# Optimization experiments

Hardware: AMD Instinct MI355X
Metric: run time of the kernel (lower is better)

The kernel has to match this reference:

```python
import jax, jax.numpy as jnp
import numpy as np

N_NODES = 100_000
N_EDGES = 3_200_000
IN_DIM, HID_DIM, EMB_DIM = 128, 64, 32


def setup_inputs() -> dict:
    key = jax.random.key(0)
    k0, k1, k2, k3, k4, k5 = jax.random.split(key, 6)
    x = jax.random.normal(k0, (N_NODES, IN_DIM), dtype=jnp.float32)
    edge_index = jax.random.randint(k1, (2, N_EDGES), 0, N_NODES, dtype=jnp.int32)
    # GCNConv parameters (glorot-ish scale)
    W1 = jax.random.normal(k2, (IN_DIM, HID_DIM), dtype=jnp.float32) / np.sqrt(IN_DIM)
    b1 = jnp.zeros((HID_DIM,), dtype=jnp.float32)
    W2 = jax.random.normal(k3, (HID_DIM, EMB_DIM), dtype=jnp.float32) / np.sqrt(HID_DIM)
    b2 = jnp.zeros((EMB_DIM,), dtype=jnp.float32)
    return {"x": x, "W1": W1, "b1": b1, "W2": W2, "b2": b2, "edge_index": edge_index}


def reference(x, W1, b1, W2, b2, edge_index):
    """Two-layer GCN encoder (PyG GCNConv semantics, eval mode so dropout is a no-op).

    Each GCNConv: add self-loops, symmetric deg^-1/2 normalization,
    out = scatter_add(norm_e * (x @ W)[src], dst) + b.
    """
    N = x.shape[0]
    loops = jnp.arange(N, dtype=edge_index.dtype)
    src = jnp.concatenate([edge_index[0], loops])  # [E+N]
    dst = jnp.concatenate([edge_index[1], loops])  # [E+N]

    # degree of destination nodes (self-loops guarantee deg >= 1)
    deg = jax.ops.segment_sum(jnp.ones_like(dst, dtype=jnp.float32), dst,
                              num_segments=N)
    dinv = jax.lax.rsqrt(deg)                      # deg^-1/2, finite since deg>=1
    norm = dinv[src] * dinv[dst]                   # [E+N]

    def gcn_conv(h, W, b):
        h = h @ W                                  # dense transform [N, D_out]
        msg = h[src] * norm[:, None]               # gather + scale [E+N, D_out]
        return jax.ops.segment_sum(msg, dst, num_segments=N) + b

    h = jax.nn.relu(gcn_conv(x, W1, b1))
    # F.dropout with training=False is identity -> omitted
    return gcn_conv(h, W2, b2)
```

## Files before the change

kernel.cpp:

```cpp
#include <hip/hip_runtime.h>

static constexpr int NN = 100000;
static constexpr int NE = 3200000;
static constexpr int DI = 128;
static constexpr int DH = 64;
static constexpr int DO = 32;

static constexpr int NBK  = 391;
static constexpr int BCAP = 9216;
static constexpr int TILE = 4096;
static constexpr int NEB  = (NE + TILE - 1) / TILE;
static constexpr int XW1_BASE = NEB + 1;
static constexpr int XW1_BLOCKS = (NN + 63) / 64;

typedef short short8 __attribute__((ext_vector_type(8)));
typedef float f32x4  __attribute__((ext_vector_type(4)));

__device__ __forceinline__ unsigned short f2bf(float f) {
    union { float f; unsigned u; } v; v.f = f;
    unsigned r = v.u + 0x7FFFu + ((v.u >> 16) & 1u);
    return (unsigned short)(r >> 16);
}
__device__ __forceinline__ float bflo(unsigned u) {
    union { unsigned u; float f; } v; v.u = u << 16; return v.f;
}
__device__ __forceinline__ float bfhi(unsigned u) {
    union { unsigned u; float f; } v; v.u = u & 0xFFFF0000u; return v.f;
}

__global__ void k_zero(int* __restrict__ p, int n) {
    int i = blockIdx.x * blockDim.x + threadIdx.x;
    if (i < n) p[i] = 0;
}

__global__ __launch_bounds__(256) void k_mega(
        const int* __restrict__ src, const int* __restrict__ dst,
        int* __restrict__ bcur, int* __restrict__ bstore,
        const float* __restrict__ x, const float* __restrict__ W1,
        const float* __restrict__ W2,
        unsigned short* __restrict__ w2bf, unsigned short* __restrict__ h1b) {
    __shared__ int hist[NBK];
    __shared__ int lcur[NBK];
    __shared__ int gpos[NBK];
    __shared__ int stage[TILE];
    __shared__ unsigned short bid[TILE];

    int tid = threadIdx.x;

    if (blockIdx.x < NEB) {
        for (int i = tid; i < NBK; i += 256) hist[i] = 0;
        __syncthreads();

        int base = blockIdx.x * TILE;
        int rem = NE - base;
        int p[16]; unsigned short bb[16];
#pragma unroll
        for (int k4 = 0; k4 < 4; ++k4) {
            int off = tid * 16 + k4 * 4;
            if (off < rem) {
                int4 s4 = *(const int4*)(src + base + off);
                int4 d4 = *(const int4*)(dst + base + off);
                int k = 4 * k4;
                bb[k + 0] = (unsigned short)((unsigned)d4.x >> 8);
                p [k + 0] = ((d4.x & 255) << 24) | s4.x;
                atomicAdd(&hist[bb[k + 0]], 1);
                bb[k + 1] = (unsigned short)((unsigned)d4.y >> 8);
                p [k + 1] = ((d4.y & 255) << 24) | s4.y;
                atomicAdd(&hist[bb[k + 1]], 1);
                bb[k + 2] = (unsigned short)((unsigned)d4.z >> 8);
                p [k + 2] = ((d4.z & 255) << 24) | s4.z;
                atomicAdd(&hist[bb[k + 2]], 1);
                bb[k + 3] = (unsigned short)((unsigned)d4.w >> 8);
                p [k + 3] = ((d4.w & 255) << 24) | s4.w;
                atomicAdd(&hist[bb[k + 3]], 1);
            } else {
                int k = 4 * k4;
                bb[k + 0] = 0xFFFF; bb[k + 1] = 0xFFFF;
                bb[k + 2] = 0xFFFF; bb[k + 3] = 0xFFFF;
            }
        }
        __syncthreads();

        for (int i = tid; i < NBK; i += 256)
            gpos[i] = atomicAdd(&bcur[i], hist[i]);
        __syncthreads();

        if (tid < 64) {
            int carry = 0;
            for (int c = 0; c < (NBK + 63) / 64; ++c) {
                int idx = c * 64 + tid;
                int v = (idx < NBK) ? hist[idx] : 0;
                int inc = v;
#pragma unroll
                for (int o = 1; o < 64; o <<= 1) {
                    int u = __shfl_up(inc, o, 64);
                    if (tid >= o) inc += u;
                }
                int tot = __shfl(inc, 63, 64);
                if (idx < NBK) { int ex = carry + inc - v; hist[idx] = ex; lcur[idx] = ex; }
                carry += tot;
            }
        }
        __syncthreads();

#pragma unroll
        for (int k = 0; k < 16; ++k) {
            if (bb[k] != 0xFFFF) {
                int lp = atomicAdd(&lcur[bb[k]], 1);
                stage[lp] = p[k];
                bid[lp] = bb[k];
            }
        }
        __syncthreads();

        int tcnt = min(TILE, rem);
        for (int i = tid; i < tcnt; i += 256) {
            int b = bid[i];
            int off = gpos[b] + (i - hist[b]);
            if (off < BCAP) bstore[b * BCAP + off] = stage[i];
        }
    } else if (blockIdx.x == NEB) {
        for (int i = tid; i < DH * DO; i += 256) w2bf[i] = f2bf(W2[i]);
    } else {
        int wave = tid >> 6, lane = tid & 63;
        int q = lane >> 4, m = lane & 15, o0 = wave * 16;
        int nb = (blockIdx.x - XW1_BASE) * 64;

        short8 bfr[4];
#pragma unroll
        for (int kb = 0; kb < 4; ++kb)
#pragma unroll
            for (int j = 0; j < 8; ++j)
                bfr[kb][j] = (short)f2bf(W1[(kb * 32 + q * 8 + j) * DH + o0 + m]);

#pragma unroll
        for (int mt = 0; mt < 4; ++mt) {
            int row = min(nb + mt * 16 + m, NN - 1);
            const float* xr = x + (size_t)row * DI;
            f32x4 acc = {0.f, 0.f, 0.f, 0.f};
#pragma unroll
            for (int kb = 0; kb < 4; ++kb) {
                f32x4 u0 = *(const f32x4*)(xr + kb * 32 + q * 8);
                f32x4 u1 = *(const f32x4*)(xr + kb * 32 + q * 8 + 4);
                short8 a;
                a[0] = (short)f2bf(u0.x); a[1] = (short)f2bf(u0.y);
                a[2] = (short)f2bf(u0.z); a[3] = (short)f2bf(u0.w);
                a[4] = (short)f2bf(u1.x); a[5] = (short)f2bf(u1.y);
                a[6] = (short)f2bf(u1.z); a[7] = (short)f2bf(u1.w);
                acc = __builtin_amdgcn_mfma_f32_16x16x32_bf16(a, bfr[kb], acc, 0, 0, 0);
            }
#pragma unroll
            for (int r = 0; r < 4; ++r) {
                int n = nb + mt * 16 + q * 4 + r;
                if (n < NN) h1b[(size_t)n * DH + o0 + m] = f2bf(acc[r]);
            }
        }
    }
}

__global__ __launch_bounds__(512) void k_bsort(
        const int* __restrict__ bcur, int* __restrict__ bstore,
        int* __restrict__ rpb, int* __restrict__ rpe, float* __restrict__ dinv,
        unsigned* __restrict__ h1) {
    __shared__ int buf[BCAP];
    __shared__ int sorted[BCAP];
    __shared__ int hist[256], scan[256], cur[256];
    __shared__ float sdinv[256];

    int b = blockIdx.x, tid = threadIdx.x;
    int cnt = min(bcur[b], BCAP);
    int base = b * BCAP;
    for (int i = tid; i < cnt; i += 512) buf[i] = bstore[base + i];
    if (tid < 256) hist[tid] = 0;
    __syncthreads();
    for (int i = tid; i < cnt; i += 512)
        atomicAdd(&hist[((unsigned)buf[i]) >> 24], 1);
    __syncthreads();

    if (tid < 64) {
        int carry = 0;
        for (int c = 0; c < 4; ++c) {
            int idx = c * 64 + tid;
            int v = hist[idx];
            int inc = v;
#pragma unroll
            for (int o = 1; o < 64; o <<= 1) {
                int u = __shfl_up(inc, o, 64);
                if (tid >= o) inc += u;
            }
            int tot = __shfl(inc, 63, 64);
            scan[idx] = carry + inc - v;
            cur[idx]  = carry + inc - v;
            carry += tot;
        }
    }
    __syncthreads();

    if (tid < 256) {
        int n = b * 256 + tid;
        if (n < NN) {
            int beg = base + scan[tid];
            rpb[n] = beg;
            rpe[n] = beg + hist[tid];
            float dv = rsqrtf(1.0f + (float)hist[tid]);
            dinv[n] = dv;
            sdinv[tid] = dv;
        }
    }

    for (int i = tid; i < cnt; i += 512) {
        unsigned pv = (unsigned)buf[i];
        int pos = atomicAdd(&cur[pv >> 24], 1);
        sorted[pos] = (int)(pv & 0xFFFFFF);
    }
    __syncthreads();
    for (int i = tid; i < cnt; i += 512) bstore[base + i] = sorted[i];

    for (int i = tid; i < 2048; i += 512) {
        int r = i >> 3, n = b * 256 + r;
        if (n < NN) {
            float dv = sdinv[r];
            uint4* p = (uint4*)h1 + (size_t)b * 2048 + i;
            uint4 u = *p;
            u.x = (unsigned)f2bf(bflo(u.x) * dv) | ((unsigned)f2bf(bfhi(u.x) * dv) << 16);
            u.y = (unsigned)f2bf(bflo(u.y) * dv) | ((unsigned)f2bf(bfhi(u.y) * dv) << 16);
            u.z = (unsigned)f2bf(bflo(u.z) * dv) | ((unsigned)f2bf(bfhi(u.z) * dv) << 16);
            u.w = (unsigned)f2bf(bflo(u.w) * dv) | ((unsigned)f2bf(bfhi(u.w) * dv) << 16);
            *p = u;
        }
    }
}

__global__ __launch_bounds__(256) void k_gather64(
        const int* __restrict__ rpb, const int* __restrict__ rpe,
        const int* __restrict__ csr, const unsigned* __restrict__ h,
        const float* __restrict__ dinv, const float* __restrict__ b1,
        unsigned* __restrict__ tbf) {
    int wave = threadIdx.x >> 6, lane = threadIdx.x & 63;
    int q = lane >> 4, f4 = lane & 15;
    int n = blockIdx.x * 4 + wave;
    int beg = rpb[n], end = rpe[n];
    float dn = dinv[n];

    float s0 = 0.f, s1 = 0.f, s2 = 0.f, s3 = 0.f;
    if (q == 0) {
        uint2 u = *(const uint2*)(h + (size_t)n * 32 + 2 * f4);
        s0 = bflo(u.x); s1 = bfhi(u.x); s2 = bflo(u.y); s3 = bfhi(u.y);
    }
    for (int c = beg; c < end; c += 64) {
        int cnt = min(64, end - c);
        int sidx = (lane < cnt) ? csr[c + lane] : 0;
        int j = 0;
        for (; j + 16 <= cnt; j += 16) {
            int sa = __shfl(sidx, j + q, 64);
            int sb = __shfl(sidx, j + 4 + q, 64);
            int sc = __shfl(sidx, j + 8 + q, 64);
            int sd = __shfl(sidx, j + 12 + q, 64);
            uint2 ua = *(const uint2*)(h + (size_t)sa * 32 + 2 * f4);
            uint2 ub = *(const uint2*)(h + (size_t)sb * 32 + 2 * f4);
            uint2 uc = *(const uint2*)(h + (size_t)sc * 32 + 2 * f4);
            uint2 ud = *(const uint2*)(h + (size_t)sd * 32 + 2 * f4);
            s0 += bflo(ua.x); s1 += bfhi(ua.x); s2 += bflo(ua.y); s3 += bfhi(ua.y);
            s0 += bflo(ub.x); s1 += bfhi(ub.x); s2 += bflo(ub.y); s3 += bfhi(ub.y);
            s0 += bflo(uc.x); s1 += bfhi(uc.x); s2 += bflo(uc.y); s3 += bfhi(uc.y);
            s0 += bflo(ud.x); s1 += bfhi(ud.x); s2 += bflo(ud.y); s3 += bfhi(ud.y);
        }
        for (; j + 8 <= cnt; j += 8) {
            int sa = __shfl(sidx, j + q, 64);
            int sb = __shfl(sidx, j + 4 + q, 64);
            uint2 ua = *(const uint2*)(h + (size_t)sa * 32 + 2 * f4);
            uint2 ub = *(const uint2*)(h + (size_t)sb * 32 + 2 * f4);
            s0 += bflo(ua.x); s1 += bfhi(ua.x); s2 += bflo(ua.y); s3 += bfhi(ua.y);
            s0 += bflo(ub.x); s1 += bfhi(ub.x); s2 += bflo(ub.y); s3 += bfhi(ub.y);
        }
        for (; j < cnt; j += 4) {
            int slot = j + q;
            int s = __shfl(sidx, slot, 64);
            if (slot < cnt) {
                uint2 u = *(const uint2*)(h + (size_t)s * 32 + 2 * f4);
                s0 += bflo(u.x); s1 += bfhi(u.x); s2 += bflo(u.y); s3 += bfhi(u.y);
            }
        }
    }
    s0 += __shfl_xor(s0, 32, 64); s1 += __shfl_xor(s1, 32, 64);
    s2 += __shfl_xor(s2, 32, 64); s3 += __shfl_xor(s3, 32, 64);
    s0 += __shfl_xor(s0, 16, 64); s1 += __shfl_xor(s1, 16, 64);
    s2 += __shfl_xor(s2, 16, 64); s3 += __shfl_xor(s3, 16, 64);
    if (q == 0) {
        float t0 = fmaxf(fmaf(s0, dn, b1[4 * f4 + 0]), 0.f);
        float t1 = fmaxf(fmaf(s1, dn, b1[4 * f4 + 1]), 0.f);
        float t2 = fmaxf(fmaf(s2, dn, b1[4 * f4 + 2]), 0.f);
        float t3 = fmaxf(fmaf(s3, dn, b1[4 * f4 + 3]), 0.f);
        uint2 o;
        o.x = (unsigned)f2bf(t0) | ((unsigned)f2bf(t1) << 16);
        o.y = (unsigned)f2bf(t2) | ((unsigned)f2bf(t3) << 16);
        *(uint2*)(tbf + (size_t)n * 32 + 2 * f4) = o;
    }
}

__global__ __launch_bounds__(256) void k_l2_mfma(
        const unsigned short* __restrict__ tbf, const unsigned short* __restrict__ w2bf,
        const float* __restrict__ dinv, unsigned short* __restrict__ h2b) {
    int wave = threadIdx.x >> 6, lane = threadIdx.x & 63;
    int q = lane >> 4, m = lane & 15;
    int o0 = (wave & 1) * 16, mt = wave >> 1;
    int nb = blockIdx.x * 32;

    short8 bf[2];
#pragma unroll
    for (int kb = 0; kb < 2; ++kb)
#pragma unroll
        for (int j = 0; j < 8; ++j)
            bf[kb][j] = (short)w2bf[(kb * 32 + q * 8 + j) * DO + o0 + m];

    int row = nb + mt * 16 + m;
    f32x4 acc = {0.f, 0.f, 0.f, 0.f};
#pragma unroll
    for (int kb = 0; kb < 2; ++kb) {
        short8 a = *(const short8*)(tbf + (size_t)row * DH + kb * 32 + q * 8);
        acc = __builtin_amdgcn_mfma_f32_16x16x32_bf16(a, bf[kb], acc, 0, 0, 0);
    }
#pragma unroll
    for (int r = 0; r < 4; ++r) {
        int n = nb + mt * 16 + q * 4 + r;
        if (n < NN) h2b[(size_t)n * DO + o0 + m] = f2bf(acc[r] * dinv[n]);
    }
}

__global__ __launch_bounds__(256) void k_gather32(
        const int* __restrict__ rpb, const int* __restrict__ rpe,
        const int* __restrict__ csr, const unsigned* __restrict__ h,
        const float* __restrict__ dinv, const float* __restrict__ b2,
        float* __restrict__ out) {
    int wave = threadIdx.x >> 6, lane = threadIdx.x & 63;
    int q = lane >> 3, f4 = lane & 7;
    int n = blockIdx.x * 4 + wave;
    int beg = rpb[n], end = rpe[n];

    float s0 = 0.f, s1 = 0.f, s2 = 0.f, s3 = 0.f;
    if (q == 0) {
        uint2 u = *(const uint2*)(h + (size_t)n * 16 + 2 * f4);
        s0 = bflo(u.x); s1 = bfhi(u.x); s2 = bflo(u.y); s3 = bfhi(u.y);
    }
    for (int c = beg; c < end; c += 64) {
        int cnt = min(64, end - c);
        int sidx = (lane < cnt) ? csr[c + lane] : 0;
        int j = 0;
        for (; j + 16 <= cnt; j += 16) {
            int sa = __shfl(sidx, j + q, 64);
            int sb = __shfl(sidx, j + 8 + q, 64);
            uint2 ua = *(const uint2*)(h + (size_t)sa * 16 + 2 * f4);
            uint2 ub = *(const uint2*)(h + (size_t)sb * 16 + 2 * f4);
            s0 += bflo(ua.x); s1 += bfhi(ua.x); s2 += bflo(ua.y); s3 += bfhi(ua.y);
            s0 += bflo(ub.x); s1 += bfhi(ub.x); s2 += bflo(ub.y); s3 += bfhi(ub.y);
        }
        for (; j < cnt; j += 8) {
            int slot = j + q;
            int s = __shfl(sidx, slot, 64);
            if (slot < cnt) {
                uint2 u = *(const uint2*)(h + (size_t)s * 16 + 2 * f4);
                s0 += bflo(u.x); s1 += bfhi(u.x); s2 += bflo(u.y); s3 += bfhi(u.y);
            }
        }
    }
    s0 += __shfl_xor(s0, 32, 64); s1 += __shfl_xor(s1, 32, 64);
    s2 += __shfl_xor(s2, 32, 64); s3 += __shfl_xor(s3, 32, 64);
    s0 += __shfl_xor(s0, 16, 64); s1 += __shfl_xor(s1, 16, 64);
    s2 += __shfl_xor(s2, 16, 64); s3 += __shfl_xor(s3, 16, 64);
    s0 += __shfl_xor(s0, 8, 64);  s1 += __shfl_xor(s1, 8, 64);
    s2 += __shfl_xor(s2, 8, 64);  s3 += __shfl_xor(s3, 8, 64);
    if (q == 0) {
        float dn = dinv[n];
        size_t o = (size_t)n * 32 + 4 * f4;
        out[o + 0] = fmaf(s0, dn, b2[4 * f4 + 0]);
        out[o + 1] = fmaf(s1, dn, b2[4 * f4 + 1]);
        out[o + 2] = fmaf(s2, dn, b2[4 * f4 + 2]);
        out[o + 3] = fmaf(s3, dn, b2[4 * f4 + 3]);
    }
}

extern "C" void kernel_launch(void* const* d_in, const int* in_sizes, int n_in,
                              void* d_out, int out_size, void* d_ws, size_t ws_size,
                              hipStream_t stream) {
    const float* x  = (const float*)d_in[0];
    const float* W1 = (const float*)d_in[1];
    const float* b1 = (const float*)d_in[2];
    const float* W2 = (const float*)d_in[3];
    const float* b2 = (const float*)d_in[4];
    const int* ei  = (const int*)d_in[5];
    const int* src = ei;
    const int* dst = ei + NE;
    float* out = (float*)d_out;

    float* ws    = (float*)d_ws;
    int*   rpb   = (int*)ws;
    int*   rpe   = (int*)(ws + 100352);
    float* dinv  = ws + 200704;
    int*   bcur  = (int*)(ws + 301056);
    int*   bstor = (int*)(ws + 301568);
    unsigned short* w2bf = (unsigned short*)(ws + 3905024);
    unsigned short* tbf  = (unsigned short*)(ws + 3906048);
    unsigned short* h1b  = (unsigned short*)(ws + 7106048);
    unsigned short* h2b  = h1b;

    k_zero     <<<2, 256, 0, stream>>>(bcur, 512);
    k_mega     <<<XW1_BASE + XW1_BLOCKS, 256, 0, stream>>>(
                    src, dst, bcur, bstor, x, W1, W2, w2bf, h1b);
    k_bsort    <<<NBK, 512, 0, stream>>>(bcur, bstor, rpb, rpe, dinv,
                                         (unsigned*)h1b);

    k_gather64 <<<NN / 4, 256, 0, stream>>>(rpb, rpe, bstor, (const unsigned*)h1b,
                                            dinv, b1, (unsigned*)tbf);
    k_l2_mfma  <<<NN / 32, 256, 0, stream>>>(tbf, w2bf, dinv, h2b);
    k_gather32 <<<NN / 4, 256, 0, stream>>>(rpb, rpe, bstor, (const unsigned*)h2b,
                                            dinv, b2, out);
}
```

Before: 277.1 us.

## Replace global atomic bucket offsets with count-scan pass for deterministic scatter

Adds a counting kernel that builds per-tile bucket histograms and a scan kernel that turns them into exclusive per-tile offsets and per-bucket totals. The mega kernel then reads its bucket offsets instead of doing global atomicAdd on bucket cursors, and the zeroing kernel is removed. This removes global atomic contention and gives a deterministic edge order inside buckets, at the cost of reading dst a second time and two extra launches.

```diff
diff --git a/kernel.cpp b/kernel.cpp
--- a/kernel.cpp
+++ b/kernel.cpp
@@ -10,6 +10,7 @@
 static constexpr int BCAP = 9216;
 static constexpr int TILE = 4096;
 static constexpr int NEB  = (NE + TILE - 1) / TILE;
+static constexpr int NEBP = 784;
 static constexpr int XW1_BASE = NEB + 1;
 static constexpr int XW1_BLOCKS = (NN + 63) / 64;
 
@@ -28,14 +29,55 @@
     union { unsigned u; float f; } v; v.u = u & 0xFFFF0000u; return v.f;
 }
 
-__global__ void k_zero(int* __restrict__ p, int n) {
-    int i = blockIdx.x * blockDim.x + threadIdx.x;
-    if (i < n) p[i] = 0;
+__global__ __launch_bounds__(256) void k_count(
+        const int* __restrict__ dst, int* __restrict__ cnt) {
+    __shared__ int hist[NBK];
+    int tid = threadIdx.x;
+    for (int i = tid; i < NBK; i += 256) hist[i] = 0;
+    __syncthreads();
+
+    int base = blockIdx.x * TILE;
+    int rem = NE - base;
+#pragma unroll
+    for (int k4 = 0; k4 < 4; ++k4) {
+        int off = tid * 16 + k4 * 4;
+        if (off < rem) {
+            int4 d4 = *(const int4*)(dst + base + off);
+            atomicAdd(&hist[(unsigned)d4.x >> 8], 1);
+            atomicAdd(&hist[(unsigned)d4.y >> 8], 1);
+            atomicAdd(&hist[(unsigned)d4.z >> 8], 1);
+            atomicAdd(&hist[(unsigned)d4.w >> 8], 1);
+        }
+    }
+    __syncthreads();
+    for (int i = tid; i < NBK; i += 256)
+        cnt[i * NEBP + blockIdx.x] = hist[i];
+}
+
+__global__ __launch_bounds__(64) void k_scan(
+        int* __restrict__ cnt, int* __restrict__ bcur) {
+    int b = blockIdx.x, tid = threadIdx.x;
+    int* row = cnt + b * NEBP;
+    int carry = 0;
+    for (int c = 0; c < (NEB + 63) / 64; ++c) {
+        int idx = c * 64 + tid;
+        int v = (idx < NEB) ? row[idx] : 0;
+        int inc = v;
+#pragma unroll
+        for (int o = 1; o < 64; o <<= 1) {
+            int u = __shfl_up(inc, o, 64);
+            if (tid >= o) inc += u;
+        }
+        int tot = __shfl(inc, 63, 64);
+        if (idx < NEB) row[idx] = carry + inc - v;
+        carry += tot;
+    }
+    if (tid == 0) bcur[b] = carry;
 }
 
 __global__ __launch_bounds__(256) void k_mega(
         const int* __restrict__ src, const int* __restrict__ dst,
-        int* __restrict__ bcur, int* __restrict__ bstore,
+        const int* __restrict__ gposM, int* __restrict__ bstore,
         const float* __restrict__ x, const float* __restrict__ W1,
         const float* __restrict__ W2,
         unsigned short* __restrict__ w2bf, unsigned short* __restrict__ h1b) {
@@ -82,7 +124,7 @@
         __syncthreads();
 
         for (int i = tid; i < NBK; i += 256)
-            gpos[i] = atomicAdd(&bcur[i], hist[i]);
+            gpos[i] = gposM[i * NEBP + blockIdx.x];
         __syncthreads();
 
         if (tid < 64) {
@@ -402,10 +444,12 @@
     unsigned short* tbf  = (unsigned short*)(ws + 3906048);
     unsigned short* h1b  = (unsigned short*)(ws + 7106048);
     unsigned short* h2b  = h1b;
-
-    k_zero     <<<2, 256, 0, stream>>>(bcur, 512);
+    int*   cntM  = (int*)tbf;
+
+    k_count    <<<NEB, 256, 0, stream>>>(dst, cntM);
+    k_scan     <<<NBK, 64, 0, stream>>>(cntM, bcur);
     k_mega     <<<XW1_BASE + XW1_BLOCKS, 256, 0, stream>>>(
-                    src, dst, bcur, bstor, x, W1, W2, w2bf, h1b);
+                    src, dst, cntM, bstor, x, W1, W2, w2bf, h1b);
     k_bsort    <<<NBK, 512, 0, stream>>>(bcur, bstor, rpb, rpe, dinv,
                                          (unsigned*)h1b);
 
```

After: 275.2 us. Within noise of the previous version (-0.7%).
